# Performance work log

Hardware: AMD Instinct MI355X
Metric: run time of the kernel (lower is better)

The kernel has to match this reference:

```python
import jax, jax.numpy as jnp
import numpy as np

B, T = 32, 2000
H = 512          # hidden_size
NH = 100         # n_harmonics
NM = 65          # n_magnitudes
E = 16           # energy_state dim
HH = 256         # hypernetwork hidden


def _lin_init(k, out_d, in_d):
    return jax.random.normal(k, (out_d, in_d), jnp.float32) / np.sqrt(in_d)


def setup_inputs() -> dict:
    key = jax.random.key(0)
    ks = jax.random.split(key, 24)
    inp = {
        'f0_scaled': jax.random.uniform(ks[0], (B, T), jnp.float32),
        'loudness': jax.random.uniform(ks[1], (B, T), jnp.float32),
        'energy_state': jax.random.normal(ks[2], (B, E), jnp.float32),
        # base decoder params
        'pre_W': _lin_init(ks[3], H, 2), 'pre_b': jnp.zeros((H,), jnp.float32),
        'W_ih': _lin_init(ks[4], 3 * H, H), 'W_hh': _lin_init(ks[5], 3 * H, H),
        'b_ih': jnp.zeros((3 * H,), jnp.float32), 'b_hh': jnp.zeros((3 * H,), jnp.float32),
        'post_W': _lin_init(ks[6], H, H), 'post_b': jnp.zeros((H,), jnp.float32),
        'harm_W': _lin_init(ks[7], NH, H), 'harm_b': jnp.zeros((NH,), jnp.float32),
        'noise_W': _lin_init(ks[8], NM, H), 'noise_b': jnp.zeros((NM,), jnp.float32),
        # hypernetwork params (small output scale so deltas are perturbative)
        'hyp_W1': _lin_init(ks[9], HH, E), 'hyp_b1': jnp.zeros((HH,), jnp.float32),
        'hyp_Wdh': _lin_init(ks[10], NH * H, HH) * 0.05, 'hyp_bdh': jnp.zeros((NH * H,), jnp.float32),
        'hyp_Wbh': _lin_init(ks[11], NH, HH) * 0.05, 'hyp_bbh': jnp.zeros((NH,), jnp.float32),
        'hyp_Wdn': _lin_init(ks[12], NM * H, HH) * 0.05, 'hyp_bdn': jnp.zeros((NM * H,), jnp.float32),
        'hyp_Wbn': _lin_init(ks[13], NM, HH) * 0.05, 'hyp_bbn': jnp.zeros((NM,), jnp.float32),
    }
    return inp


def _gru(x, W_ih, W_hh, b_ih, b_hh):
    # x: [B,T,H] -> [B,T,H], torch nn.GRU cell equations
    gi = jnp.einsum('bth,gh->btg', x, W_ih) + b_ih  # [B,T,3H]
    gi = jnp.swapaxes(gi, 0, 1)  # [T,B,3H]
    h0 = jnp.zeros((x.shape[0], W_hh.shape[1]), x.dtype)

    def step(h, gi_t):
        gh = h @ W_hh.T + b_hh
        ir, iz, in_ = jnp.split(gi_t, 3, axis=-1)
        hr, hz, hn = jnp.split(gh, 3, axis=-1)
        r = jax.nn.sigmoid(ir + hr)
        z = jax.nn.sigmoid(iz + hz)
        n = jnp.tanh(in_ + r * hn)
        h_new = (1.0 - z) * n + z * h
        return h_new, h_new

    _, ys = jax.lax.scan(step, h0, gi)
    return jnp.swapaxes(ys, 0, 1)  # [B,T,H]


def reference(f0_scaled, loudness, energy_state,
              pre_W, pre_b, W_ih, W_hh, b_ih, b_hh, post_W, post_b,
              harm_W, harm_b, noise_W, noise_b,
              hyp_W1, hyp_b1, hyp_Wdh, hyp_bdh, hyp_Wbh, hyp_bbh,
              hyp_Wdn, hyp_bdn, hyp_Wbn, hyp_bbn):
    Bs = energy_state.shape[0]
    # Hypernetwork: energy_state -> per-batch weight/bias deltas
    h = jax.nn.relu(energy_state @ hyp_W1.T + hyp_b1)            # [B,HH]
    dW_harm = (h @ hyp_Wdh.T + hyp_bdh).reshape(Bs, NH, H)
    db_harm = h @ hyp_Wbh.T + hyp_bbh                            # [B,NH]
    dW_noise = (h @ hyp_Wdn.T + hyp_bdn).reshape(Bs, NM, H)
    db_noise = h @ hyp_Wbn.T + hyp_bbn                           # [B,NM]

    # Base decoder trunk
    x = jnp.stack([f0_scaled, loudness], axis=-1)                # [B,T,2]
    x = jax.nn.leaky_relu(jnp.einsum('bti,hi->bth', x, pre_W) + pre_b)
    x = _gru(x, W_ih, W_hh, b_ih, b_hh)
    x = jax.nn.leaky_relu(jnp.einsum('bth,oh->bto', x, post_W) + post_b)

    # Modulated heads: per-batch effective weight shared across T (no [B*T,O,H] blow-up)
    eff_hW = harm_W[None] + dW_harm                              # [B,NH,H]
    eff_hb = harm_b[None] + db_harm                              # [B,NH]
    harm_out = jnp.einsum('bth,boh->bto', x, eff_hW) + eff_hb[:, None, :]
    harmonic_amps = jax.nn.sigmoid(harm_out)                     # [B,T,NH]

    eff_nW = noise_W[None] + dW_noise                            # [B,NM,H]
    eff_nb = noise_b[None] + db_noise                            # [B,NM]
    noise_out = jnp.einsum('bth,boh->bto', x, eff_nW) + eff_nb[:, None, :]
    noise_mags = jax.nn.sigmoid(noise_out)                       # [B,T,NM]
    return harmonic_amps, noise_mags
```

## Files before the change

kernel.cpp:

```cpp
#include <hip/hip_runtime.h>
#include <hip/hip_fp16.h>
#include <stdint.h>

#define B_  32
#define T_  2000
#define H_  512
#define NH_ 100
#define NM_ 65

typedef _Float16 f16x8 __attribute__((ext_vector_type(8)));
typedef _Float16 f16x2 __attribute__((ext_vector_type(2)));
typedef float    f32x4 __attribute__((ext_vector_type(4)));

typedef __attribute__((address_space(3))) void lds_void_t;
typedef __attribute__((address_space(1))) void glb_void_t;

__device__ __forceinline__ void gload_lds16(const void* g, void* l) {
  __builtin_amdgcn_global_load_lds((const glb_void_t*)g, (lds_void_t*)l, 16, 0, 0);
}

__device__ __forceinline__ float sigmoidf_(float x) {
  float e = __builtin_amdgcn_exp2f(-x * 1.44269504f);
  return __builtin_amdgcn_rcpf(1.0f + e);
}
__device__ __forceinline__ float tanhf_(float x) {
  float e = __builtin_amdgcn_exp2f(x * 2.88539008f);
  return 1.0f - 2.0f * __builtin_amdgcn_rcpf(e + 1.0f);
}
__device__ __forceinline__ float dot2(unsigned w, unsigned h, float acc) {
  return __builtin_amdgcn_fdot2(__builtin_bit_cast(f16x2, w),
                                __builtin_bit_cast(f16x2, h), acc, false);
}
__device__ __forceinline__ unsigned pack2(float a, float b) {
  __half2 h = __floats2half2_rn(a, b);
  return __builtin_bit_cast(unsigned, h);
}
__device__ __forceinline__ float hsel(unsigned w, int hi) {
  __half2 h2 = __builtin_bit_cast(__half2, w);
  return hi ? __high2float(h2) : __low2float(h2);
}
__device__ __forceinline__ int hq_swz(int i) {
  int cs = i >> 5, kk = (i >> 2) & 7;
  return cs*32 + ((kk ^ cs) << 2) + (i & 3);
}

__global__ void hyper1(const float* __restrict__ es, const float* __restrict__ W1,
                       const float* __restrict__ b1, float* __restrict__ hE) {
  int b = blockIdx.x, o = threadIdx.x;
  float a = b1[o];
  #pragma unroll
  for (int c = 0; c < 16; ++c) a += es[b*16 + c] * W1[o*16 + c];
  hE[b*256 + o] = fmaxf(a, 0.f);
}

__global__ void hyper2(const float* __restrict__ hE,
                       const float* __restrict__ Wbh, const float* __restrict__ bbh,
                       const float* __restrict__ harmb,
                       const float* __restrict__ Wbn, const float* __restrict__ bbn,
                       const float* __restrict__ noiseb, float* __restrict__ effb) {
  int b = blockIdx.x, o = threadIdx.x;
  if (o < NH_) {
    float a = bbh[o] + harmb[o];
    for (int c = 0; c < 256; ++c) a += hE[b*256 + c] * Wbh[o*256 + c];
    effb[b*256 + o] = a;
  } else if (o < NH_ + NM_) {
    int q = o - NH_;
    float a = bbn[q] + noiseb[q];
    for (int c = 0; c < 256; ++c) a += hE[b*256 + c] * Wbn[q*256 + c];
    effb[b*256 + o] = a;
  }
}

__global__ __launch_bounds__(256) void hyper3(
    const float* __restrict__ hE, const float* __restrict__ Wd,
    const float* __restrict__ bd, const float* __restrict__ baseW,
    __half* __restrict__ effW, int o_base) {
  __shared__ float wl[256*33];
  __shared__ float hEl[32*256];
  int tid = threadIdx.x;
  int row0 = blockIdx.x * 256;
  #pragma unroll
  for (int i = 0; i < 32; ++i) hEl[i*256 + tid] = hE[i*256 + tid];
  float acc[32];
  #pragma unroll
  for (int b = 0; b < 32; ++b) acc[b] = 0.f;
  for (int cc = 0; cc < 256; cc += 32) {
    __syncthreads();
    #pragma unroll
    for (int i = 0; i < 32; ++i) {
      int idx = i*256 + tid;
      int r = idx >> 5, c = idx & 31;
      wl[r*33 + c] = Wd[(size_t)(row0 + r)*256 + cc + c];
    }
    __syncthreads();
    #pragma unroll
    for (int c = 0; c < 32; ++c) {
      float w = wl[tid*33 + c];
      #pragma unroll
      for (int b = 0; b < 32; ++b) acc[b] += w * hEl[b*256 + cc + c];
    }
  }
  int row = row0 + tid;
  int o = row >> 9, h = row & 511;
  float base = baseW[row] + bd[row];
  #pragma unroll
  for (int b = 0; b < 32; ++b) {
    effW[((size_t)b*256 + o_base + o)*512 + h] = (__half)(acc[b] + base);
  }
}

__global__ void cvt_f16(const float* __restrict__ in, __half* __restrict__ out, int n) {
  int i = blockIdx.x*256 + threadIdx.x;
  if (i < n) out[i] = (__half)in[i];
}

__global__ void pack_whh4(const float* __restrict__ Whh, uint4* __restrict__ Wp) {
  int idx = blockIdx.x*256 + threadIdx.x;
  int t = idx % 384;
  int k = (idx / 384) & 31;
  int w = idx / (384*32);
  int rq = t >> 3, cs = t & 7;
  int j = k >> 3, kk = k & 7;
  int row = (rq >> 4)*512 + w*64 + (rq & 15)*4 + j;
  int col0 = cs*64 + kk*8;
  const float* src = Whh + (size_t)row*512 + col0;
  uint4 o;
  o.x = pack2(src[0], src[1]);
  o.y = pack2(src[2], src[3]);
  o.z = pack2(src[4], src[5]);
  o.w = pack2(src[6], src[7]);
  Wp[idx] = o;
}

__global__ void pre_kernel(const float* __restrict__ f0, const float* __restrict__ loud,
                           const float* __restrict__ preW, const float* __restrict__ preb,
                           __half* __restrict__ xpre, int CH, int c0) {
  int b = blockIdx.y;
  int idx = blockIdx.x*256 + threadIdx.x;
  int t = idx >> 9, h = idx & 511;
  int mg = b*T_ + c0 + t;
  float v = f0[mg]*preW[h*2+0] + loud[mg]*preW[h*2+1] + preb[h];
  v = v >= 0.f ? v : 0.01f*v;
  xpre[((size_t)b*CH + t)*512 + h] = (__half)v;
}

template<int ACT>
__global__ __launch_bounds__(256) void gemm_nt(
    const __half* __restrict__ A, const __half* __restrict__ B,
    __half* __restrict__ C, const float* __restrict__ bias, int N) {
  constexpr int K = 512;
  __shared__ __align__(16) __half As[128*64];
  __shared__ __align__(16) __half Bs[128*64];
  int tid = threadIdx.x;
  int bx = blockIdx.x, by = blockIdx.y;
  const __half* Ab = A + (size_t)bx*128*K;
  const __half* Bb = B + (size_t)by*128*K;
  f32x4 acc[4][4] = {};
  int lane = tid & 63;
  int wv = tid >> 6, wr = wv >> 1, wc = wv & 1;
  int lr = lane & 15, lk = lane >> 4;

  for (int kt = 0; kt < K/64; ++kt) {
    #pragma unroll
    for (int j = 0; j < 4; ++j) {
      int idx = j*256 + tid;
      int row = idx >> 3, seg = idx & 7;
      const __half* gpA = Ab + (size_t)row*K + kt*64 + seg*8;
      const __half* gpB = Bb + (size_t)row*K + kt*64 + seg*8;
      __half* lpA = As + (size_t)(j*256 + (tid & ~63))*8;
      __half* lpB = Bs + (size_t)(j*256 + (tid & ~63))*8;
      gload_lds16(gpA, lpA);
      gload_lds16(gpB, lpB);
    }
    __syncthreads();
    #pragma unroll
    for (int ks = 0; ks < 2; ++ks) {
      f16x8 af[4], bf[4];
      #pragma unroll
      for (int i = 0; i < 4; ++i)
        af[i] = *(const f16x8*)(As + (wr*64 + i*16 + lr)*64 + ks*32 + lk*8);
      #pragma unroll
      for (int j2 = 0; j2 < 4; ++j2)
        bf[j2] = *(const f16x8*)(Bs + (wc*64 + j2*16 + lr)*64 + ks*32 + lk*8);
      #pragma unroll
      for (int i = 0; i < 4; ++i)
        #pragma unroll
        for (int j2 = 0; j2 < 4; ++j2)
          acc[i][j2] = __builtin_amdgcn_mfma_f32_16x16x32_f16(af[i], bf[j2], acc[i][j2], 0, 0, 0);
    }
    __syncthreads();
  }

  #pragma unroll
  for (int j2 = 0; j2 < 4; ++j2) {
    int col = by*128 + wc*64 + j2*16 + lr;
    float bv = bias[col];
    #pragma unroll
    for (int i = 0; i < 4; ++i) {
      int row0 = bx*128 + wr*64 + i*16 + lk*4;
      #pragma unroll
      for (int r = 0; r < 4; ++r) {
        float v = acc[i][j2][r] + bv;
        if (ACT == 1) v = v >= 0.f ? v : 0.01f*v;
        C[(size_t)(row0 + r)*N + col] = (__half)v;
      }
    }
  }
}

__global__ __launch_bounds__(256) void heads_gemm(
    const __half* __restrict__ Apc, const __half* __restrict__ effW,
    const float* __restrict__ effb, float* __restrict__ out, int CH, int c0) {
  constexpr int K = 512;
  __shared__ __align__(16) __half As[128*64];
  __shared__ __align__(16) __half Bs[128*64];
  int tid = threadIdx.x;
  int bx = blockIdx.x, by = blockIdx.y, b = blockIdx.z;
  const __half* Ab = Apc + (size_t)b*CH*K;
  const __half* Bb = effW + ((size_t)b*256 + (size_t)by*128)*K;
  f32x4 acc[4][4] = {};
  int lane = tid & 63;
  int wv = tid >> 6, wr = wv >> 1, wc = wv & 1;
  int lr = lane & 15, lk = lane >> 4;

  for (int kt = 0; kt < K/64; ++kt) {
    #pragma unroll
    for (int j = 0; j < 4; ++j) {
      int idx = j*256 + tid;
      int row = idx >> 3, seg = idx & 7;
      int ar = bx*128 + row; if (ar > CH-1) ar = CH-1;
      const __half* gpA = Ab + (size_t)ar*K + kt*64 + seg*8;
      const __half* gpB = Bb + (size_t)row*K + kt*64 + seg*8;
      __half* lpA = As + (size_t)(j*256 + (tid & ~63))*8;
      __half* lpB = Bs + (size_t)(j*256 + (tid & ~63))*8;
      gload_lds16(gpA, lpA);
      gload_lds16(gpB, lpB);
    }
    __syncthreads();
    #pragma unroll
    for (int ks = 0; ks < 2; ++ks) {
      f16x8 af[4], bf[4];
      #pragma unroll
      for (int i = 0; i < 4; ++i)
        af[i] = *(const f16x8*)(As + (wr*64 + i*16 + lr)*64 + ks*32 + lk*8);
      #pragma unroll
      for (int j2 = 0; j2 < 4; ++j2)
        bf[j2] = *(const f16x8*)(Bs + (wc*64 + j2*16 + lr)*64 + ks*32 + lk*8);
      #pragma unroll
      for (int i = 0; i < 4; ++i)
        #pragma unroll
        for (int j2 = 0; j2 < 4; ++j2)
          acc[i][j2] = __builtin_amdgcn_mfma_f32_16x16x32_f16(af[i], bf[j2], acc[i][j2], 0, 0, 0);
    }
    __syncthreads();
  }

  #pragma unroll
  for (int j2 = 0; j2 < 4; ++j2) {
    int o = by*128 + wc*64 + j2*16 + lr;
    if (o < NH_ + NM_) {
      float bv = effb[b*256 + o];
      #pragma unroll
      for (int i = 0; i < 4; ++i) {
        #pragma unroll
        for (int r = 0; r < 4; ++r) {
          int trow = bx*128 + wr*64 + i*16 + lk*4 + r;
          if (trow < CH) {
            int tg = c0 + trow;
            float v = sigmoidf_(acc[i][j2][r] + bv);
            if (o < NH_)
              out[((size_t)b*T_ + tg)*NH_ + o] = v;
            else
              out[(size_t)B_*T_*NH_ + ((size_t)b*T_ + tg)*NM_ + (o - NH_)] = v;
          }
        }
      }
    }
  }
}

#define LOADW(k) { const uint4* p = Wp + ((size_t)(w*32 + (k)))*384 + t; \
  asm volatile("global_load_dwordx4 %0, %1, off" : "=v"(wq_##k) : "v"(p) : "memory"); }

#define DOT4(k, hv, A) { \
  A = dot2(wq_##k.x, hv.x, A); A = dot2(wq_##k.y, hv.y, A); \
  A = dot2(wq_##k.z, hv.z, A); A = dot2(wq_##k.w, hv.w, A); }

#define BARX() do { asm volatile("s_waitcnt lgkmcnt(0)\n\ts_barrier" ::: "memory"); \
                    __builtin_amdgcn_sched_barrier(0); } while (0)

__global__ __launch_bounds__(512) __attribute__((amdgpu_waves_per_eu(2, 4)))
void gru_scan8(
    const uint4* __restrict__ Wp, const __half* __restrict__ gi_c,
    const float* __restrict__ bhh, __half* __restrict__ ys_c,
    float* __restrict__ hstate, unsigned long long* __restrict__ xch64,
    int CH, int first) {
  int wg = blockIdx.x;
  int b = wg & 31;
  int w = wg >> 5;
  int t = threadIdx.x;
  int rq = t >> 3, cs = t & 7;
  bool wact = (t < 384);
  bool comb = (t >= 384 && t < 416);
  int tc = t - 384;

  __shared__ __align__(16) unsigned hq[256];
  __shared__ float part[192];
  __shared__ float gil[192];

  uint4 wq_0{},wq_1{},wq_2{},wq_3{},wq_4{},wq_5{},wq_6{},wq_7{},
        wq_8{},wq_9{},wq_10{},wq_11{},wq_12{},wq_13{},wq_14{},wq_15{},
        wq_16{},wq_17{},wq_18{},wq_19{},wq_20{},wq_21{},wq_22{},wq_23{},
        wq_24{},wq_25{},wq_26{},wq_27{},wq_28{},wq_29{},wq_30{},wq_31{};
  if (wact) {
    LOADW(0)  LOADW(1)  LOADW(2)  LOADW(3)  LOADW(4)  LOADW(5)  LOADW(6)  LOADW(7)
    LOADW(8)  LOADW(9)  LOADW(10) LOADW(11) LOADW(12) LOADW(13) LOADW(14) LOADW(15)
    LOADW(16) LOADW(17) LOADW(18) LOADW(19) LOADW(20) LOADW(21) LOADW(22) LOADW(23)
    LOADW(24) LOADW(25) LOADW(26) LOADW(27) LOADW(28) LOADW(29) LOADW(30) LOADW(31)
  }
  asm volatile("s_waitcnt vmcnt(0)" ::: "memory");
  __builtin_amdgcn_sched_barrier(0);

  float br0=0.f,br1=0.f,bz0=0.f,bz1=0.f,bn0=0.f,bn1=0.f;
  if (comb) {
    int u0 = w*64 + 2*tc;
    br0 = bhh[u0];        br1 = bhh[u0+1];
    bz0 = bhh[512+u0];    bz1 = bhh[512+u0+1];
    bn0 = bhh[1024+u0];   bn1 = bhh[1024+u0+1];
  }

  if (t < 256) {
    unsigned hv0 = first ? 0u : pack2(hstate[b*512 + 2*t], hstate[b*512 + 2*t + 1]);
    hq[hq_swz(t)] = hv0;
  }
  __syncthreads();

  const __half* gib = gi_c + (size_t)b*CH*1536;
  __half* ysb = ys_c + (size_t)b*CH*512;
  const uint4* hq4 = (const uint4*)hq;
  int hb = cs*8;

  float giv_cur = 0.f, giv_next = 0.f;
  if (t < 192) giv_cur = (float)gib[(t >> 6)*512 + w*64 + (t & 63)];

  for (int s = 0; s < CH; ++s) {
    int p = s & 1;
    unsigned long long* xp64 = xch64 + ((size_t)p*32 + b)*256;

    if (t < 192 && s + 1 < CH)
      giv_next = (float)gib[(size_t)(s+1)*1536 + (t >> 6)*512 + w*64 + (t & 63)];

    if (wact) {
      uint4 hv0_ = hq4[hb + (0 ^ cs)];
      uint4 hv1_ = hq4[hb + (1 ^ cs)];
      uint4 hv2_ = hq4[hb + (2 ^ cs)];
      uint4 hv3_ = hq4[hb + (3 ^ cs)];
      uint4 hv4_ = hq4[hb + (4 ^ cs)];
      uint4 hv5_ = hq4[hb + (5 ^ cs)];
      uint4 hv6_ = hq4[hb + (6 ^ cs)];
      uint4 hv7_ = hq4[hb + (7 ^ cs)];
      float a0 = 0.f, a1 = 0.f, a2 = 0.f, a3 = 0.f;
      DOT4(0,hv0_,a0)  DOT4(8,hv0_,a1)  DOT4(16,hv0_,a2) DOT4(24,hv0_,a3)
      DOT4(1,hv1_,a0)  DOT4(9,hv1_,a1)  DOT4(17,hv1_,a2) DOT4(25,hv1_,a3)
      DOT4(2,hv2_,a0)  DOT4(10,hv2_,a1) DOT4(18,hv2_,a2) DOT4(26,hv2_,a3)
      DOT4(3,hv3_,a0)  DOT4(11,hv3_,a1) DOT4(19,hv3_,a2) DOT4(27,hv3_,a3)
      DOT4(4,hv4_,a0)  DOT4(12,hv4_,a1) DOT4(20,hv4_,a2) DOT4(28,hv4_,a3)
      DOT4(5,hv5_,a0)  DOT4(13,hv5_,a1) DOT4(21,hv5_,a2) DOT4(29,hv5_,a3)
      DOT4(6,hv6_,a0)  DOT4(14,hv6_,a1) DOT4(22,hv6_,a2) DOT4(30,hv6_,a3)
      DOT4(7,hv7_,a0)  DOT4(15,hv7_,a1) DOT4(23,hv7_,a2) DOT4(31,hv7_,a3)
      a0 += __shfl_xor(a0, 1); a0 += __shfl_xor(a0, 2); a0 += __shfl_xor(a0, 4);
      a1 += __shfl_xor(a1, 1); a1 += __shfl_xor(a1, 2); a1 += __shfl_xor(a1, 4);
      a2 += __shfl_xor(a2, 1); a2 += __shfl_xor(a2, 2); a2 += __shfl_xor(a2, 4);
      a3 += __shfl_xor(a3, 1); a3 += __shfl_xor(a3, 2); a3 += __shfl_xor(a3, 4);
      if (cs < 4) {
        float v = (cs == 0) ? a0 : (cs == 1) ? a1 : (cs == 2) ? a2 : a3;
        part[(rq << 2) + cs] = v;
      }
      if (t < 192) gil[t] = giv_cur;
    }
    giv_cur = giv_next;
    BARX();

    if (comb) {
      int j0 = 2*tc, j1 = 2*tc + 1;
      float r0 = sigmoidf_(gil[j0] + part[j0] + br0);
      float r1 = sigmoidf_(gil[j1] + part[j1] + br1);
      float z0 = sigmoidf_(gil[64+j0] + part[64+j0] + bz0);
      float z1 = sigmoidf_(gil[64+j1] + part[64+j1] + bz1);
      float n0 = tanhf_(gil[128+j0] + r0*(part[128+j0] + bn0));
      float n1 = tanhf_(gil[128+j1] + r1*(part[128+j1] + bn1));
      int gidx = w*32 + tc;
      int hidx = hq_swz(gidx);
      unsigned hold = hq[hidx];
      float h0 = (1.f - z0)*n0 + z0*hsel(hold, 0);
      float h1 = (1.f - z1)*n1 + z1*hsel(hold, 1);
      unsigned hv = pack2(h0, h1);
      hq[hidx] = hv;
      *(unsigned*)&ysb[(size_t)s*512 + w*64 + j0] = hv;
      unsigned long long tv = ((unsigned long long)(unsigned)(s + 1) << 32)
                              | (unsigned long long)hv;
      __hip_atomic_store(&xp64[gidx], tv,
                         __ATOMIC_RELAXED, __HIP_MEMORY_SCOPE_AGENT);
      if (s == CH - 1) {
        hstate[b*512 + w*64 + j0] = h0;
        hstate[b*512 + w*64 + j1] = h1;
      }
    } else if (t < 256 && (t >> 5) != w) {
      unsigned long long v;
      do {
        v = __hip_atomic_load(&xp64[t], __ATOMIC_RELAXED, __HIP_MEMORY_SCOPE_AGENT);
      } while ((unsigned)(v >> 32) != (unsigned)(s + 1));
      hq[hq_swz(t)] = (unsigned)v;
    }
    BARX();
  }
}

extern "C" void kernel_launch(void* const* d_in, const int* in_sizes, int n_in,
                              void* d_out, int out_size, void* d_ws, size_t ws_size,
                              hipStream_t stream) {
  const float* f0     = (const float*)d_in[0];
  const float* loud   = (const float*)d_in[1];
  const float* es     = (const float*)d_in[2];
  const float* preW   = (const float*)d_in[3];
  const float* preb   = (const float*)d_in[4];
  const float* Wih    = (const float*)d_in[5];
  const float* Whh    = (const float*)d_in[6];
  const float* b_ih   = (const float*)d_in[7];
  const float* b_hh   = (const float*)d_in[8];
  const float* postW  = (const float*)d_in[9];
  const float* postb  = (const float*)d_in[10];
  const float* harmW  = (const float*)d_in[11];
  const float* harmb  = (const float*)d_in[12];
  const float* noiseW = (const float*)d_in[13];
  const float* noiseb = (const float*)d_in[14];
  const float* hypW1  = (const float*)d_in[15];
  const float* hypb1  = (const float*)d_in[16];
  const float* Wdh    = (const float*)d_in[17];
  const float* bdh    = (const float*)d_in[18];
  const float* Wbh    = (const float*)d_in[19];
  const float* bbh    = (const float*)d_in[20];
  const float* Wdn    = (const float*)d_in[21];
  const float* bdn    = (const float*)d_in[22];
  const float* Wbn    = (const float*)d_in[23];
  const float* bbn    = (const float*)d_in[24];
  (void)in_sizes; (void)n_in; (void)out_size;

  const size_t FIXED = 13312ull*1024ull;
  int CH = 20;
  {
    const int opts[8] = {2000, 1000, 500, 400, 200, 100, 40, 20};
    for (int i = 0; i < 8; ++i) {
      size_t need = FIXED + (size_t)opts[i] * 163840ull + 65536ull;
      if (need <= ws_size) { CH = opts[i]; break; }
    }
  }
  const int NC = T_ / CH;
  const int Mc = B_ * CH;

  char* w = (char*)d_ws;
  size_t off = 0;
  auto alloc = [&](size_t bytes) -> void* {
    void* p = (void*)(w + off);
    off += (bytes + 255) & ~(size_t)255;
    return p;
  };
  float*    hE      = (float*)alloc((size_t)32*256*4);
  float*    effb    = (float*)alloc((size_t)32*256*4);
  float*    hstate  = (float*)alloc((size_t)32*512*4);
  __half*   effW    = (__half*)alloc((size_t)32*256*512*2);
  __half*   Wih16   = (__half*)alloc((size_t)1536*512*2);
  __half*   postW16 = (__half*)alloc((size_t)512*512*2);
  uint4*    Wp      = (uint4*)alloc((size_t)8*32*384*16 + 4096);
  unsigned long long* xch64 = (unsigned long long*)alloc((size_t)2*32*256*8);
  __half*   xpre    = (__half*)alloc((size_t)Mc*512*2);
  __half*   gibuf   = (__half*)alloc((size_t)Mc*1536*2);
  __half*   ysbuf   = (__half*)alloc((size_t)Mc*512*2);
  __half*   postc   = xpre;

  hyper1<<<32, 256, 0, stream>>>(es, hypW1, hypb1, hE);
  hyper2<<<32, 256, 0, stream>>>(hE, Wbh, bbh, harmb, Wbn, bbn, noiseb, effb);
  hyper3<<<200, 256, 0, stream>>>(hE, Wdh, bdh, harmW, effW, 0);
  hyper3<<<130, 256, 0, stream>>>(hE, Wdn, bdn, noiseW, effW, NH_);
  cvt_f16<<<(1536*512)/256, 256, 0, stream>>>(Wih, Wih16, 1536*512);
  cvt_f16<<<(512*512)/256, 256, 0, stream>>>(postW, postW16, 512*512);
  pack_whh4<<<384, 256, 0, stream>>>(Whh, Wp);

  for (int c = 0; c < NC; ++c) {
    int c0 = c * CH;
    pre_kernel<<<dim3(CH*2, 32), 256, 0, stream>>>(f0, loud, preW, preb, xpre, CH, c0);
    gemm_nt<0><<<dim3(Mc/128, 12), 256, 0, stream>>>(xpre, Wih16, gibuf, b_ih, 1536);
    gru_scan8<<<256, 512, 0, stream>>>(Wp, gibuf, b_hh, ysbuf, hstate, xch64,
                                       CH, c == 0 ? 1 : 0);
    gemm_nt<1><<<dim3(Mc/128, 4), 256, 0, stream>>>(ysbuf, postW16, postc, postb, 512);
    heads_gemm<<<dim3((CH+127)/128, 2, 32), 256, 0, stream>>>(postc, effW, effb,
                                                              (float*)d_out, CH, c0);
  }
}
```

Before: 4.267 ms.

## Assign GRU scan roles by XCC locality and add fast L2 exchange path

Each workgroup reads its XCC and CU id and claims a (batch, slice) role through atomic CAS. The eight workgroups that share a batch therefore tend to land on the same XCC and can exchange hidden state through that XCC's L2. A second exchange buffer is written with plain stores and polled with sc0 loads, and the device-scope atomic path stays as a fallback. A large dummy LDS array limits each CU to one workgroup so the roles spread across CUs. Tags now carry a global step index, so they stay distinct across chunks. The cost is an extra zeroing launch per chunk, a claim-loop prologue, and dependence on undocumented hardware register fields and on cache behaviour.

```diff
diff --git a/kernel.cpp b/kernel.cpp
--- a/kernel.cpp
+++ b/kernel.cpp
@@ -113,6 +113,8 @@
   int i = blockIdx.x*256 + threadIdx.x;
   if (i < n) out[i] = (__half)in[i];
 }
+
+__global__ void zero_claims(unsigned* __restrict__ c) { c[threadIdx.x] = 0u; }
 
 __global__ void pack_whh4(const float* __restrict__ Whh, uint4* __restrict__ Wp) {
   int idx = blockIdx.x*256 + threadIdx.x;
@@ -294,11 +296,31 @@
     const uint4* __restrict__ Wp, const __half* __restrict__ gi_c,
     const float* __restrict__ bhh, __half* __restrict__ ys_c,
     float* __restrict__ hstate, unsigned long long* __restrict__ xch64,
-    int CH, int first) {
-  int wg = blockIdx.x;
-  int b = wg & 31;
-  int w = wg >> 5;
+    unsigned long long* __restrict__ xfl2, unsigned* __restrict__ claim,
+    int CH, int first, int tb) {
   int t = threadIdx.x;
+
+  __shared__ unsigned pad[20480];
+  __shared__ int role_sh;
+  if (first > 1) pad[t] = t;
+
+  if (t == 0) {
+    unsigned xcc, hwid;
+    asm volatile("s_getreg_b32 %0, hwreg(HW_REG_XCC_ID)" : "=s"(xcc));
+    asm volatile("s_getreg_b32 %0, hwreg(HW_REG_HW_ID)" : "=s"(hwid));
+    int base = (int)(xcc & 7) * 32;
+    int cu = (int)((hwid >> 8) & 0xF) | (int)(((hwid >> 12) & 1) << 4);
+    int role = 0;
+    for (int i = 0; i < 288; ++i) {
+      int sidx = (i < 32) ? base + ((cu + i) & 31) : (base + i) & 255;
+      if (atomicCAS(&claim[sidx], 0u, 1u) == 0u) { role = sidx; break; }
+    }
+    role_sh = role;
+  }
+  __syncthreads();
+  int role = role_sh;
+  int b = role >> 3;
+  int w = role & 7;
   int rq = t >> 3, cs = t & 7;
   bool wact = (t < 384);
   bool comb = (t >= 384 && t < 416);
@@ -346,6 +368,8 @@
   for (int s = 0; s < CH; ++s) {
     int p = s & 1;
     unsigned long long* xp64 = xch64 + ((size_t)p*32 + b)*256;
+    unsigned long long* xf   = xfl2  + ((size_t)p*32 + b)*256;
+    unsigned tag = (unsigned)(tb + s + 1);
 
     if (t < 192 && s + 1 < CH)
       giv_next = (float)gib[(size_t)(s+1)*1536 + (t >> 6)*512 + w*64 + (t & 63)];
@@ -395,21 +419,32 @@
       float h0 = (1.f - z0)*n0 + z0*hsel(hold, 0);
       float h1 = (1.f - z1)*n1 + z1*hsel(hold, 1);
       unsigned hv = pack2(h0, h1);
-      hq[hidx] = hv;
+      unsigned* fsl = (unsigned*)&xf[gidx];
+      asm volatile("global_store_dword %0, %1, off" :: "v"(fsl), "v"(hv) : "memory");
       *(unsigned*)&ysb[(size_t)s*512 + w*64 + j0] = hv;
-      unsigned long long tv = ((unsigned long long)(unsigned)(s + 1) << 32)
-                              | (unsigned long long)hv;
+      asm volatile("s_waitcnt vmcnt(0)" ::: "memory");
+      asm volatile("global_store_dword %0, %1, off" :: "v"(fsl + 1), "v"(tag) : "memory");
+      unsigned long long tv = ((unsigned long long)tag << 32) | (unsigned long long)hv;
       __hip_atomic_store(&xp64[gidx], tv,
                          __ATOMIC_RELAXED, __HIP_MEMORY_SCOPE_AGENT);
+      hq[hidx] = hv;
       if (s == CH - 1) {
         hstate[b*512 + w*64 + j0] = h0;
         hstate[b*512 + w*64 + j1] = h1;
       }
     } else if (t < 256 && (t >> 5) != w) {
       unsigned long long v;
-      do {
-        v = __hip_atomic_load(&xp64[t], __ATOMIC_RELAXED, __HIP_MEMORY_SCOPE_AGENT);
-      } while ((unsigned)(v >> 32) != (unsigned)(s + 1));
+      int it = 0;
+      for (;;) {
+        unsigned long long fv;
+        asm volatile("global_load_dwordx2 %0, %1, off sc0\n\ts_waitcnt vmcnt(0)"
+                     : "=v"(fv) : "v"(&xf[t]) : "memory");
+        if ((unsigned)(fv >> 32) == tag) { v = fv; break; }
+        if (it++ >= 1) {
+          v = __hip_atomic_load(&xp64[t], __ATOMIC_RELAXED, __HIP_MEMORY_SCOPE_AGENT);
+          if ((unsigned)(v >> 32) == tag) break;
+        }
+      }
       hq[hq_swz(t)] = (unsigned)v;
     }
     BARX();
@@ -446,7 +481,7 @@
   const float* bbn    = (const float*)d_in[24];
   (void)in_sizes; (void)n_in; (void)out_size;
 
-  const size_t FIXED = 13312ull*1024ull;
+  const size_t FIXED = 15360ull*1024ull;
   int CH = 20;
   {
     const int opts[8] = {2000, 1000, 500, 400, 200, 100, 40, 20};
@@ -473,6 +508,8 @@
   __half*   postW16 = (__half*)alloc((size_t)512*512*2);
   uint4*    Wp      = (uint4*)alloc((size_t)8*32*384*16 + 4096);
   unsigned long long* xch64 = (unsigned long long*)alloc((size_t)2*32*256*8);
+  unsigned long long* xfl2  = (unsigned long long*)alloc((size_t)2*32*256*8);
+  unsigned* claim   = (unsigned*)alloc((size_t)256*4);
   __half*   xpre    = (__half*)alloc((size_t)Mc*512*2);
   __half*   gibuf   = (__half*)alloc((size_t)Mc*1536*2);
   __half*   ysbuf   = (__half*)alloc((size_t)Mc*512*2);
@@ -490,8 +527,9 @@
     int c0 = c * CH;
     pre_kernel<<<dim3(CH*2, 32), 256, 0, stream>>>(f0, loud, preW, preb, xpre, CH, c0);
     gemm_nt<0><<<dim3(Mc/128, 12), 256, 0, stream>>>(xpre, Wih16, gibuf, b_ih, 1536);
-    gru_scan8<<<256, 512, 0, stream>>>(Wp, gibuf, b_hh, ysbuf, hstate, xch64,
-                                       CH, c == 0 ? 1 : 0);
+    zero_claims<<<1, 256, 0, stream>>>(claim);
+    gru_scan8<<<256, 512, 0, stream>>>(Wp, gibuf, b_hh, ysbuf, hstate, xch64, xfl2,
+                                       claim, CH, c == 0 ? 1 : 0, c*CH);
     gemm_nt<1><<<dim3(Mc/128, 4), 256, 0, stream>>>(ysbuf, postW16, postc, postb, 512);
     heads_gemm<<<dim3((CH+127)/128, 2, 32), 256, 0, stream>>>(postc, effW, effb,
                                                               (float*)d_out, CH, c0);
```

Result: slower. 4.536 ms (+6.3%).
